# Performance work log

Hardware: AMD Instinct MI355X
Metric: run time of the kernel (lower is better)

The kernel has to match this reference:

```python
import jax, jax.numpy as jnp
import numpy as np

TIMESCALE = 10.0   # NeuralODE init kwarg
N_MAX = 48         # static upper bound on number of constant-size Dopri5 steps
B, D, H = 8192, 128, 128


def _mlp(y, W1, b1, W2, b2):
    # autonomous dynamics f(x): tanh MLP, applied along last dim
    return jnp.tanh(y @ W1 + b1) @ W2 + b2


def _dopri5_step(y, dt, f):
    # classic Dormand-Prince 5(4) tableau; autonomous f, so c_i unused
    k1 = f(y)
    k2 = f(y + dt * (1.0 / 5.0 * k1))
    k3 = f(y + dt * (3.0 / 40.0 * k1 + 9.0 / 40.0 * k2))
    k4 = f(y + dt * (44.0 / 45.0 * k1 - 56.0 / 15.0 * k2 + 32.0 / 9.0 * k3))
    k5 = f(y + dt * (19372.0 / 6561.0 * k1 - 25360.0 / 2187.0 * k2
                     + 64448.0 / 6561.0 * k3 - 212.0 / 729.0 * k4))
    k6 = f(y + dt * (9017.0 / 3168.0 * k1 - 355.0 / 33.0 * k2
                     + 46732.0 / 5247.0 * k3 + 49.0 / 176.0 * k4
                     - 5103.0 / 18656.0 * k5))
    return y + dt * (35.0 / 384.0 * k1 + 500.0 / 1113.0 * k3
                     + 125.0 / 192.0 * k4 - 2187.0 / 6784.0 * k5
                     + 11.0 / 84.0 * k6)


def _initial_step_size(y0, f0, f, order=4, rtol=1.4e-8, atol=1.4e-8):
    # faithful port of NeuralODE.initial_step_size (Hairer heuristic)
    scale = atol + jnp.abs(y0) * rtol
    d0 = jnp.linalg.norm(y0 / scale)
    d1 = jnp.linalg.norm(f0 / scale)
    h0 = jnp.where((d0 < 1e-5) | (d1 < 1e-5), 1e-6, 0.01 * d0 / d1)
    y1 = y0 + h0 * f0
    f1 = f(y1)
    d2 = jnp.linalg.norm((f1 - f0) / scale) / h0
    h1 = jnp.where((d1 <= 1e-15) & (d2 <= 1e-15),
                   jnp.maximum(1e-6, h0 * 1e-3),
                   (0.01 / (d1 + d2)) ** (1.0 / (order + 1.0)))
    return jnp.minimum(100.0 * h0, h1)


def setup_inputs() -> dict:
    key = jax.random.key(0)
    k0, k1, k2 = jax.random.split(key, 3)
    x = jax.random.normal(k0, (B, D), jnp.float32)
    W1 = jax.random.normal(k1, (D, H), jnp.float32) * (1.0 / D ** 0.5)
    b1 = jnp.zeros((H,), jnp.float32)
    W2 = jax.random.normal(k2, (H, D), jnp.float32) * (1.0 / H ** 0.5)
    b2 = jnp.zeros((D,), jnp.float32)
    t = jnp.ones((1,), jnp.float32)
    return {"t": t, "x": x, "W1": W1, "b1": b1, "W2": W2, "b2": b2}


def reference(t, x, W1, b1, W2, b2):
    f = lambda y: _mlp(y, W1, b1, W2, b2)
    # dt0 from the first state row, exactly as the original (x[0, :])
    dt0 = _initial_step_size(x[0], f(x[0]), f)
    T = t[0] / TIMESCALE  # linspace(0, t/timescale, 2) -> ts = [0, T]

    # diffrax default ConstantStepSize: fixed-dt Dopri5 until t reaches T.
    # Static-length scan with dt clamped to the remaining interval; once
    # t == T, dt == 0 and the step is skipped via lax.cond.
    step = jax.checkpoint(
        lambda y, dt: jax.lax.cond(dt > 0.0,
                                   lambda a: _dopri5_step(a, dt, f),
                                   lambda a: a, y))

    def body(carry, _):
        tt, y = carry
        dt = jnp.clip(T - tt, 0.0, dt0)
        return (tt + dt, step(y, dt)), None

    (_, yT), _ = jax.lax.scan(body, (jnp.zeros((), jnp.float32), x), None,
                              length=N_MAX)
    # SaveAt(ts=[0, T]) -> ys has leading axis n_samples=2
    return jnp.stack([x, yT])
```

## Files before the change

kernel.cpp:

```cpp
#include <hip/hip_runtime.h>


typedef __attribute__((ext_vector_type(8))) short short8;
typedef __attribute__((ext_vector_type(4))) float f32x4;

#define SL 136

__device__ __forceinline__ short f2bf(float f) {
  union { float f; unsigned u; } v; v.f = f;
  return (short)((v.u + 0x8000u) >> 16);
}

__device__ __forceinline__ float fast_tanh(float x) {
  float e = __builtin_amdgcn_exp2f(x * 2.88539008177793f);
  float r = __builtin_amdgcn_rcpf(e + 1.0f);
  return __builtin_fmaf(-2.0f, r, 1.0f);
}

__device__ __forceinline__ void store_bf16_pair(short* p0, short* p1,
                                                float a, float b) {
  unsigned u;
  asm("v_cvt_pk_bf16_f32 %0, %1, %2" : "=v"(u) : "v"(a), "v"(b));
  *p0 = (short)(u & 0xffffu);
  *p1 = (short)(u >> 16);
}

__global__ __launch_bounds__(256, 2)
void node_kernel(const float* __restrict__ tptr, const float* __restrict__ x,
                 const float* __restrict__ W1, const float* __restrict__ b1,
                 const float* __restrict__ W2, const float* __restrict__ b2,
                 float* __restrict__ out) {
  const int tid  = threadIdx.x;
  const int wv   = tid >> 6;
  const int lane = tid & 63;
  const int q    = lane >> 4;
  const int colL = lane & 15;
  const int blockRow = blockIdx.x * 16;

  __shared__ short A1[16][SL];
  __shared__ short A2[16][SL];
  __shared__ float sred[256];

  short8 w1f[2][4], w2f[2][4];
  float b1v[2], b2v[2];
  int ncol[2];
#pragma unroll
  for (int j = 0; j < 2; ++j) {
    const int n = (2 * wv + j) * 16 + colL;
    ncol[j] = n;
    b1v[j] = b1[n]; b2v[j] = b2[n];
#pragma unroll
    for (int kt = 0; kt < 4; ++kt) {
      short8 v1, v2;
#pragma unroll
      for (int i = 0; i < 8; ++i) {
        const int k = kt * 32 + q * 8 + i;
        v1[i] = f2bf(W1[k * 128 + n]);
        v2[i] = f2bf(W2[k * 128 + n]);
      }
      w1f[j][kt] = v1; w2f[j][kt] = v2;
    }
  }

  auto block_sum = [&](float v) -> float {
    sred[tid] = v;
    __syncthreads();
    if (tid < 64) {
      float s = sred[tid] + sred[tid + 64] + sred[tid + 128] + sred[tid + 192];
#pragma unroll
      for (int o = 32; o > 0; o >>= 1) s += __shfl_down(s, o, 64);
      if (tid == 0) sred[0] = s;
    }
    __syncthreads();
    float r = sred[0];
    __syncthreads();
    return r;
  };

  short* const wr1 = &A1[q * 4][0];
  short* const wr2 = &A2[q * 4][0];
  const short* const rd1 = &A1[colL][q * 8];
  const short* const rd2 = &A2[colL][q * 8];

  auto evalF = [&](auto&& gen, f32x4 (&fout)[2]) {
#pragma unroll
    for (int j = 0; j < 2; ++j) {
      f32x4 v = gen(j);
      store_bf16_pair(&wr1[0 * SL + ncol[j]], &wr1[1 * SL + ncol[j]], v[0], v[1]);
      store_bf16_pair(&wr1[2 * SL + ncol[j]], &wr1[3 * SL + ncol[j]], v[2], v[3]);
    }
    __syncthreads();
    short8 af[4];
#pragma unroll
    for (int kt = 0; kt < 4; ++kt) af[kt] = *(const short8*)(rd1 + kt * 32);
    f32x4 acc0 = {b1v[0], b1v[0], b1v[0], b1v[0]};
    f32x4 acc1 = {b1v[1], b1v[1], b1v[1], b1v[1]};
    __builtin_amdgcn_s_setprio(1);
#pragma unroll
    for (int kt = 0; kt < 4; ++kt) {
      acc0 = __builtin_amdgcn_mfma_f32_16x16x32_bf16(af[kt], w1f[0][kt], acc0, 0, 0, 0);
      acc1 = __builtin_amdgcn_mfma_f32_16x16x32_bf16(af[kt], w1f[1][kt], acc1, 0, 0, 0);
    }
    __builtin_amdgcn_s_setprio(0);
    {
      float h0a = fast_tanh(acc0[0]), h1a = fast_tanh(acc0[1]);
      float h2a = fast_tanh(acc0[2]), h3a = fast_tanh(acc0[3]);
      store_bf16_pair(&wr2[0 * SL + ncol[0]], &wr2[1 * SL + ncol[0]], h0a, h1a);
      store_bf16_pair(&wr2[2 * SL + ncol[0]], &wr2[3 * SL + ncol[0]], h2a, h3a);
      float h0b = fast_tanh(acc1[0]), h1b = fast_tanh(acc1[1]);
      float h2b = fast_tanh(acc1[2]), h3b = fast_tanh(acc1[3]);
      store_bf16_pair(&wr2[0 * SL + ncol[1]], &wr2[1 * SL + ncol[1]], h0b, h1b);
      store_bf16_pair(&wr2[2 * SL + ncol[1]], &wr2[3 * SL + ncol[1]], h2b, h3b);
    }
    __syncthreads();
#pragma unroll
    for (int kt = 0; kt < 4; ++kt) af[kt] = *(const short8*)(rd2 + kt * 32);
    f32x4 f0 = {b2v[0], b2v[0], b2v[0], b2v[0]};
    f32x4 f1 = {b2v[1], b2v[1], b2v[1], b2v[1]};
    __builtin_amdgcn_s_setprio(1);
#pragma unroll
    for (int kt = 0; kt < 4; ++kt) {
      f0 = __builtin_amdgcn_mfma_f32_16x16x32_bf16(af[kt], w2f[0][kt], f0, 0, 0, 0);
      f1 = __builtin_amdgcn_mfma_f32_16x16x32_bf16(af[kt], w2f[1][kt], f1, 0, 0, 0);
    }
    __builtin_amdgcn_s_setprio(0);
    fout[0] = f0; fout[1] = f1;
  };

  float y0j[2], scl[2];
#pragma unroll
  for (int j = 0; j < 2; ++j) {
    y0j[j] = x[ncol[j]];
    scl[j] = 1.4e-8f + fabsf(y0j[j]) * 1.4e-8f;
  }
  f32x4 fb[2];
  evalF([&](int j) { float v = y0j[j]; return (f32x4){v, v, v, v}; }, fb);
  float f0j[2] = {fb[0][0], fb[1][0]};
  float t0 = 0.f, t1 = 0.f;
  if (q == 0) {
#pragma unroll
    for (int j = 0; j < 2; ++j) {
      float a = y0j[j] / scl[j]; t0 += a * a;
      float b = f0j[j] / scl[j]; t1 += b * b;
    }
  }
  float d0 = sqrtf(block_sum(t0));
  float d1 = sqrtf(block_sum(t1));
  float h0 = (d0 < 1e-5f || d1 < 1e-5f) ? 1e-6f : 0.01f * d0 / d1;
  evalF([&](int j) { float v = y0j[j] + h0 * f0j[j]; return (f32x4){v, v, v, v}; }, fb);
  float t2 = 0.f;
  if (q == 0) {
#pragma unroll
    for (int j = 0; j < 2; ++j) {
      float a = (fb[j][0] - f0j[j]) / scl[j]; t2 += a * a;
    }
  }
  float d2 = sqrtf(block_sum(t2)) / h0;
  float h1 = (d1 <= 1e-15f && d2 <= 1e-15f) ? fmaxf(1e-6f, h0 * 1e-3f)
                                            : powf(0.01f / (d1 + d2), 0.2f);
  const float dt0v = fminf(100.f * h0, h1);

  f32x4 yr[2];
#pragma unroll
  for (int j = 0; j < 2; ++j)
#pragma unroll
    for (int r = 0; r < 4; ++r)
      yr[j][r] = x[(blockRow + q * 4 + r) * 128 + ncol[j]];

  const float T = tptr[0] / 10.0f;
  float tt = 0.f;
  f32x4 k1[2], k2[2], k3[2], k4[2], k5[2], k6[2];

#pragma unroll 1
  for (int it = 0; it < 48; ++it) {
    float dt = fminf(fmaxf(T - tt, 0.f), dt0v);
    if (dt <= 0.f) break;
    evalF([&](int j) { return yr[j]; }, k1);
    {
      const float c1 = dt * 0.2f;
      evalF([&](int j) { return yr[j] + c1 * k1[j]; }, k2);
    }
    {
      const float c1 = dt * 0.075f, c2 = dt * 0.225f;
      evalF([&](int j) { return yr[j] + c1 * k1[j] + c2 * k2[j]; }, k3);
    }
    {
      const float c1 = dt * 0.9777777777777777f, c2 = dt * -3.7333333333333334f,
                  c3 = dt * 3.5555555555555554f;
      evalF([&](int j) { return yr[j] + c1 * k1[j] + c2 * k2[j] + c3 * k3[j]; }, k4);
    }
    {
      const float c1 = dt * 2.9525986892242035f, c2 = dt * -11.595793324188385f,
                  c3 = dt * 9.822892851699436f, c4 = dt * -0.2908093278463649f;
      evalF([&](int j) {
        return yr[j] + c1 * k1[j] + c2 * k2[j] + c3 * k3[j] + c4 * k4[j];
      }, k5);
    }
    {
      const float c1 = dt * 2.8462752525252526f, c2 = dt * -10.757575757575758f,
                  c3 = dt * 8.906422717743473f, c4 = dt * 0.2784090909090909f,
                  c5 = dt * -0.27351165254237287f;
      evalF([&](int j) {
        return yr[j] + c1 * k1[j] + c2 * k2[j] + c3 * k3[j] + c4 * k4[j]
                     + c5 * k5[j];
      }, k6);
    }
    {
      const float c1 = dt * 0.0911458333333333f, c3 = dt * 0.449236298292902f,
                  c4 = dt * 0.6510416666666666f, c5 = dt * -0.32237617924528303f,
                  c6 = dt * 0.13095238095238096f;
#pragma unroll
      for (int j = 0; j < 2; ++j)
        yr[j] = yr[j] + c1 * k1[j] + c3 * k3[j] + c4 * k4[j] + c5 * k5[j]
                      + c6 * k6[j];
    }
    tt += dt;
  }

  {
    const float4* x4 = (const float4*)(x + blockRow * 128);
    float4* o4 = (float4*)(out + blockRow * 128);
    o4[tid] = x4[tid];
    o4[tid + 256] = x4[tid + 256];
    float* oy = out + 8192 * 128;
#pragma unroll
    for (int j = 0; j < 2; ++j)
#pragma unroll
      for (int r = 0; r < 4; ++r)
        oy[(blockRow + q * 4 + r) * 128 + ncol[j]] = yr[j][r];
  }
}

extern "C" void kernel_launch(void* const* d_in, const int* in_sizes, int n_in,
                              void* d_out, int out_size, void* d_ws, size_t ws_size,
                              hipStream_t stream) {
  const float* t  = (const float*)d_in[0];
  const float* x  = (const float*)d_in[1];
  const float* W1 = (const float*)d_in[2];
  const float* b1 = (const float*)d_in[3];
  const float* W2 = (const float*)d_in[4];
  const float* b2 = (const float*)d_in[5];
  float* out = (float*)d_out;
  node_kernel<<<dim3(512), dim3(256), 0, stream>>>(t, x, W1, b1, W2, b2, out);
}
```

Measured before the change: 138.7 us.

## Pack bf16 LDS stores via lane shuffle, split MFMA chains, accumulate RK stages incrementally

LDS staging now pairs neighbouring lanes with a shuffle and byte-permute, so each lane writes packed 32-bit words instead of four separate 16-bit stores. Each K=128 MFMA reduction is split into two independent accumulator chains (low and high k-tiles) to shorten the dependent MFMA latency chain, at the cost of extra adds and registers. The Dopri5 stage combinations are restructured into running partial sums (P3..P6, Ys) updated right after each stage's k is available, with those updates placed between the LDS read and the MFMAs to overlap with latency. This also cuts live k registers from six to two buffers but adds accumulator registers.

```diff
diff --git a/kernel.cpp b/kernel.cpp
--- a/kernel.cpp
+++ b/kernel.cpp
@@ -17,12 +17,10 @@
   return __builtin_fmaf(-2.0f, r, 1.0f);
 }
 
-__device__ __forceinline__ void store_bf16_pair(short* p0, short* p1,
-                                                float a, float b) {
+__device__ __forceinline__ unsigned cvtpk(float a, float b) {
   unsigned u;
   asm("v_cvt_pk_bf16_f32 %0, %1, %2" : "=v"(u) : "v"(a), "v"(b));
-  *p0 = (short)(u & 0xffffu);
-  *p1 = (short)(u >> 16);
+  return u;
 }
 
 __global__ __launch_bounds__(256, 2)
@@ -35,6 +33,7 @@
   const int lane = tid & 63;
   const int q    = lane >> 4;
   const int colL = lane & 15;
+  const int par  = colL & 1;
   const int blockRow = blockIdx.x * 16;
 
   __shared__ short A1[16][SL];
@@ -77,54 +76,75 @@
     return r;
   };
 
-  short* const wr1 = &A1[q * 4][0];
-  short* const wr2 = &A2[q * 4][0];
+  const int rbase = q * 4 + par * 2;
+  unsigned* wA1[2]; unsigned* wA2[2];
+#pragma unroll
+  for (int j = 0; j < 2; ++j) {
+    const int nb = ncol[j] & ~1;
+    wA1[j] = (unsigned*)&A1[rbase][nb];
+    wA2[j] = (unsigned*)&A2[rbase][nb];
+  }
   const short* const rd1 = &A1[colL][q * 8];
   const short* const rd2 = &A2[colL][q * 8];
 
-  auto evalF = [&](auto&& gen, f32x4 (&fout)[2]) {
-#pragma unroll
-    for (int j = 0; j < 2; ++j) {
-      f32x4 v = gen(j);
-      store_bf16_pair(&wr1[0 * SL + ncol[j]], &wr1[1 * SL + ncol[j]], v[0], v[1]);
-      store_bf16_pair(&wr1[2 * SL + ncol[j]], &wr1[3 * SL + ncol[j]], v[2], v[3]);
-    }
+  auto stage_pair = [&](unsigned* p, f32x4 v) {
+    unsigned A = cvtpk(v[0], v[1]);
+    unsigned B = cvtpk(v[2], v[3]);
+    unsigned send = par ? A : B;
+    unsigned got = (unsigned)__shfl_xor((int)send, 1, 64);
+    unsigned losrc = par ? got : A;
+    unsigned hisrc = par ? B : got;
+    p[0] = __builtin_amdgcn_perm(hisrc, losrc, 0x05040100u);
+    *(unsigned*)((short*)p + SL) = __builtin_amdgcn_perm(hisrc, losrc, 0x07060302u);
+  };
+
+  auto evalF = [&](const f32x4 (&gin)[2], auto&& post, f32x4 (&fout)[2]) {
+    stage_pair(wA1[0], gin[0]);
+    stage_pair(wA1[1], gin[1]);
     __syncthreads();
     short8 af[4];
 #pragma unroll
     for (int kt = 0; kt < 4; ++kt) af[kt] = *(const short8*)(rd1 + kt * 32);
-    f32x4 acc0 = {b1v[0], b1v[0], b1v[0], b1v[0]};
-    f32x4 acc1 = {b1v[1], b1v[1], b1v[1], b1v[1]};
+    post();
+    f32x4 aL0 = {b1v[0], b1v[0], b1v[0], b1v[0]};
+    f32x4 aL1 = {b1v[1], b1v[1], b1v[1], b1v[1]};
+    f32x4 aH0 = {0.f, 0.f, 0.f, 0.f}, aH1 = {0.f, 0.f, 0.f, 0.f};
     __builtin_amdgcn_s_setprio(1);
-#pragma unroll
-    for (int kt = 0; kt < 4; ++kt) {
-      acc0 = __builtin_amdgcn_mfma_f32_16x16x32_bf16(af[kt], w1f[0][kt], acc0, 0, 0, 0);
-      acc1 = __builtin_amdgcn_mfma_f32_16x16x32_bf16(af[kt], w1f[1][kt], acc1, 0, 0, 0);
-    }
+    aL0 = __builtin_amdgcn_mfma_f32_16x16x32_bf16(af[0], w1f[0][0], aL0, 0, 0, 0);
+    aL1 = __builtin_amdgcn_mfma_f32_16x16x32_bf16(af[0], w1f[1][0], aL1, 0, 0, 0);
+    aH0 = __builtin_amdgcn_mfma_f32_16x16x32_bf16(af[2], w1f[0][2], aH0, 0, 0, 0);
+    aH1 = __builtin_amdgcn_mfma_f32_16x16x32_bf16(af[2], w1f[1][2], aH1, 0, 0, 0);
+    aL0 = __builtin_amdgcn_mfma_f32_16x16x32_bf16(af[1], w1f[0][1], aL0, 0, 0, 0);
+    aL1 = __builtin_amdgcn_mfma_f32_16x16x32_bf16(af[1], w1f[1][1], aL1, 0, 0, 0);
+    aH0 = __builtin_amdgcn_mfma_f32_16x16x32_bf16(af[3], w1f[0][3], aH0, 0, 0, 0);
+    aH1 = __builtin_amdgcn_mfma_f32_16x16x32_bf16(af[3], w1f[1][3], aH1, 0, 0, 0);
     __builtin_amdgcn_s_setprio(0);
-    {
-      float h0a = fast_tanh(acc0[0]), h1a = fast_tanh(acc0[1]);
-      float h2a = fast_tanh(acc0[2]), h3a = fast_tanh(acc0[3]);
-      store_bf16_pair(&wr2[0 * SL + ncol[0]], &wr2[1 * SL + ncol[0]], h0a, h1a);
-      store_bf16_pair(&wr2[2 * SL + ncol[0]], &wr2[3 * SL + ncol[0]], h2a, h3a);
-      float h0b = fast_tanh(acc1[0]), h1b = fast_tanh(acc1[1]);
-      float h2b = fast_tanh(acc1[2]), h3b = fast_tanh(acc1[3]);
-      store_bf16_pair(&wr2[0 * SL + ncol[1]], &wr2[1 * SL + ncol[1]], h0b, h1b);
-      store_bf16_pair(&wr2[2 * SL + ncol[1]], &wr2[3 * SL + ncol[1]], h2b, h3b);
-    }
+    f32x4 th0, th1;
+#pragma unroll
+    for (int r = 0; r < 4; ++r) {
+      th0[r] = fast_tanh(aL0[r] + aH0[r]);
+      th1[r] = fast_tanh(aL1[r] + aH1[r]);
+    }
+    stage_pair(wA2[0], th0);
+    stage_pair(wA2[1], th1);
     __syncthreads();
 #pragma unroll
     for (int kt = 0; kt < 4; ++kt) af[kt] = *(const short8*)(rd2 + kt * 32);
-    f32x4 f0 = {b2v[0], b2v[0], b2v[0], b2v[0]};
-    f32x4 f1 = {b2v[1], b2v[1], b2v[1], b2v[1]};
+    f32x4 fL0 = {b2v[0], b2v[0], b2v[0], b2v[0]};
+    f32x4 fL1 = {b2v[1], b2v[1], b2v[1], b2v[1]};
+    f32x4 fH0 = {0.f, 0.f, 0.f, 0.f}, fH1 = {0.f, 0.f, 0.f, 0.f};
     __builtin_amdgcn_s_setprio(1);
-#pragma unroll
-    for (int kt = 0; kt < 4; ++kt) {
-      f0 = __builtin_amdgcn_mfma_f32_16x16x32_bf16(af[kt], w2f[0][kt], f0, 0, 0, 0);
-      f1 = __builtin_amdgcn_mfma_f32_16x16x32_bf16(af[kt], w2f[1][kt], f1, 0, 0, 0);
-    }
+    fL0 = __builtin_amdgcn_mfma_f32_16x16x32_bf16(af[0], w2f[0][0], fL0, 0, 0, 0);
+    fL1 = __builtin_amdgcn_mfma_f32_16x16x32_bf16(af[0], w2f[1][0], fL1, 0, 0, 0);
+    fH0 = __builtin_amdgcn_mfma_f32_16x16x32_bf16(af[2], w2f[0][2], fH0, 0, 0, 0);
+    fH1 = __builtin_amdgcn_mfma_f32_16x16x32_bf16(af[2], w2f[1][2], fH1, 0, 0, 0);
+    fL0 = __builtin_amdgcn_mfma_f32_16x16x32_bf16(af[1], w2f[0][1], fL0, 0, 0, 0);
+    fL1 = __builtin_amdgcn_mfma_f32_16x16x32_bf16(af[1], w2f[1][1], fL1, 0, 0, 0);
+    fH0 = __builtin_amdgcn_mfma_f32_16x16x32_bf16(af[3], w2f[0][3], fH0, 0, 0, 0);
+    fH1 = __builtin_amdgcn_mfma_f32_16x16x32_bf16(af[3], w2f[1][3], fH1, 0, 0, 0);
     __builtin_amdgcn_s_setprio(0);
-    fout[0] = f0; fout[1] = f1;
+    fout[0] = fL0 + fH0;
+    fout[1] = fL1 + fH1;
   };
 
   float y0j[2], scl[2];
@@ -133,8 +153,10 @@
     y0j[j] = x[ncol[j]];
     scl[j] = 1.4e-8f + fabsf(y0j[j]) * 1.4e-8f;
   }
-  f32x4 fb[2];
-  evalF([&](int j) { float v = y0j[j]; return (f32x4){v, v, v, v}; }, fb);
+  f32x4 fb[2], gb[2];
+#pragma unroll
+  for (int j = 0; j < 2; ++j) gb[j] = (f32x4){y0j[j], y0j[j], y0j[j], y0j[j]};
+  evalF(gb, [&] {}, fb);
   float f0j[2] = {fb[0][0], fb[1][0]};
   float t0 = 0.f, t1 = 0.f;
   if (q == 0) {
@@ -147,7 +169,12 @@
   float d0 = sqrtf(block_sum(t0));
   float d1 = sqrtf(block_sum(t1));
   float h0 = (d0 < 1e-5f || d1 < 1e-5f) ? 1e-6f : 0.01f * d0 / d1;
-  evalF([&](int j) { float v = y0j[j] + h0 * f0j[j]; return (f32x4){v, v, v, v}; }, fb);
+#pragma unroll
+  for (int j = 0; j < 2; ++j) {
+    float v = y0j[j] + h0 * f0j[j];
+    gb[j] = (f32x4){v, v, v, v};
+  }
+  evalF(gb, [&] {}, fb);
   float t2 = 0.f;
   if (q == 0) {
 #pragma unroll
@@ -169,51 +196,72 @@
 
   const float T = tptr[0] / 10.0f;
   float tt = 0.f;
-  f32x4 k1[2], k2[2], k3[2], k4[2], k5[2], k6[2];
+  f32x4 kA[2], kB[2], P3[2], P4[2], P5[2], P6[2], Ys[2], g[2];
 
 #pragma unroll 1
   for (int it = 0; it < 48; ++it) {
     float dt = fminf(fmaxf(T - tt, 0.f), dt0v);
     if (dt <= 0.f) break;
-    evalF([&](int j) { return yr[j]; }, k1);
-    {
-      const float c1 = dt * 0.2f;
-      evalF([&](int j) { return yr[j] + c1 * k1[j]; }, k2);
-    }
-    {
-      const float c1 = dt * 0.075f, c2 = dt * 0.225f;
-      evalF([&](int j) { return yr[j] + c1 * k1[j] + c2 * k2[j]; }, k3);
-    }
-    {
-      const float c1 = dt * 0.9777777777777777f, c2 = dt * -3.7333333333333334f,
-                  c3 = dt * 3.5555555555555554f;
-      evalF([&](int j) { return yr[j] + c1 * k1[j] + c2 * k2[j] + c3 * k3[j]; }, k4);
-    }
-    {
-      const float c1 = dt * 2.9525986892242035f, c2 = dt * -11.595793324188385f,
-                  c3 = dt * 9.822892851699436f, c4 = dt * -0.2908093278463649f;
-      evalF([&](int j) {
-        return yr[j] + c1 * k1[j] + c2 * k2[j] + c3 * k3[j] + c4 * k4[j];
-      }, k5);
-    }
-    {
-      const float c1 = dt * 2.8462752525252526f, c2 = dt * -10.757575757575758f,
-                  c3 = dt * 8.906422717743473f, c4 = dt * 0.2784090909090909f,
-                  c5 = dt * -0.27351165254237287f;
-      evalF([&](int j) {
-        return yr[j] + c1 * k1[j] + c2 * k2[j] + c3 * k3[j] + c4 * k4[j]
-                     + c5 * k5[j];
-      }, k6);
-    }
-    {
-      const float c1 = dt * 0.0911458333333333f, c3 = dt * 0.449236298292902f,
-                  c4 = dt * 0.6510416666666666f, c5 = dt * -0.32237617924528303f,
-                  c6 = dt * 0.13095238095238096f;
-#pragma unroll
-      for (int j = 0; j < 2; ++j)
-        yr[j] = yr[j] + c1 * k1[j] + c3 * k3[j] + c4 * k4[j] + c5 * k5[j]
-                      + c6 * k6[j];
-    }
+    const float a21 = dt * 0.2f;
+    const float a31 = dt * 0.075f,              a32 = dt * 0.225f;
+    const float a41 = dt * 0.9777777777777777f, a42 = dt * -3.7333333333333334f,
+                a43 = dt * 3.5555555555555554f;
+    const float a51 = dt * 2.9525986892242035f, a52 = dt * -11.595793324188385f,
+                a53 = dt * 9.822892851699436f,  a54 = dt * -0.2908093278463649f;
+    const float a61 = dt * 2.8462752525252526f, a62 = dt * -10.757575757575758f,
+                a63 = dt * 8.906422717743473f,  a64 = dt * 0.2784090909090909f,
+                a65 = dt * -0.27351165254237287f;
+    const float bb1 = dt * 0.0911458333333333f, bb3 = dt * 0.449236298292902f,
+                bb4 = dt * 0.6510416666666666f, bb5 = dt * -0.32237617924528303f,
+                bb6 = dt * 0.13095238095238096f;
+
+    evalF(yr, [&] {
+#pragma unroll
+      for (int j = 0; j < 2; ++j) {
+        P3[j] = yr[j]; P4[j] = yr[j]; P5[j] = yr[j]; P6[j] = yr[j]; Ys[j] = yr[j];
+      }
+    }, kA);
+#pragma unroll
+    for (int j = 0; j < 2; ++j) g[j] = yr[j] + a21 * kA[j];
+    evalF(g, [&] {
+#pragma unroll
+      for (int j = 0; j < 2; ++j) {
+        P3[j] += a31 * kA[j]; P4[j] += a41 * kA[j]; P5[j] += a51 * kA[j];
+        P6[j] += a61 * kA[j]; Ys[j] += bb1 * kA[j];
+      }
+    }, kB);
+#pragma unroll
+    for (int j = 0; j < 2; ++j) g[j] = P3[j] + a32 * kB[j];
+    evalF(g, [&] {
+#pragma unroll
+      for (int j = 0; j < 2; ++j) {
+        P4[j] += a42 * kB[j]; P5[j] += a52 * kB[j]; P6[j] += a62 * kB[j];
+      }
+    }, kA);
+#pragma unroll
+    for (int j = 0; j < 2; ++j) g[j] = P4[j] + a43 * kA[j];
+    evalF(g, [&] {
+#pragma unroll
+      for (int j = 0; j < 2; ++j) {
+        P5[j] += a53 * kA[j]; P6[j] += a63 * kA[j]; Ys[j] += bb3 * kA[j];
+      }
+    }, kB);
+#pragma unroll
+    for (int j = 0; j < 2; ++j) g[j] = P5[j] + a54 * kB[j];
+    evalF(g, [&] {
+#pragma unroll
+      for (int j = 0; j < 2; ++j) {
+        P6[j] += a64 * kB[j]; Ys[j] += bb4 * kB[j];
+      }
+    }, kA);
+#pragma unroll
+    for (int j = 0; j < 2; ++j) g[j] = P6[j] + a65 * kA[j];
+    evalF(g, [&] {
+#pragma unroll
+      for (int j = 0; j < 2; ++j) Ys[j] += bb5 * kA[j];
+    }, kB);
+#pragma unroll
+    for (int j = 0; j < 2; ++j) yr[j] = Ys[j] + bb6 * kB[j];
     tt += dt;
   }
 
```

Result: slower. 148.6 us (+7.2%).
